# Kernel optimization log

Measured on AMD Instinct MI355X. Metric: run time of the kernel, lower is better.

## Reference

```python
import jax, jax.numpy as jnp
import numpy as np

B, L1, L2, D = 32, 512, 512, 1024


def setup_inputs() -> dict:
    key = jax.random.key(0)
    k1, k2, k3, k4 = jax.random.split(key, 4)
    v1 = jax.random.normal(k1, (B, L1, D), dtype=jnp.float32)
    v2 = jax.random.normal(k2, (B, L2, D), dtype=jnp.float32)
    # row/column is fully masked (which would NaN the softmax).
    v1_mask = jax.random.uniform(k3, (B, L1)) < 0.2
    v2_mask = jax.random.uniform(k4, (B, L2)) < 0.2
    return {"v1": v1, "v2": v2, "v1_mask": v1_mask, "v2_mask": v2_mask}


def reference(v1, v2, v1_mask, v2_mask):
    # similarity: [B, L1, L2]
    sim = jnp.einsum("bid,bjd->bij", v1, v2)
    neg_inf = jnp.float32(-jnp.inf)
    # softmax over v2 positions (dim=2), masking padded v2 columns
    v1_v2_attn = jax.nn.softmax(
        jnp.where(v2_mask[:, None, :], neg_inf, sim), axis=2)
    # softmax over v1 positions (dim=1), masking padded v1 rows
    v2_v1_attn = jax.nn.softmax(
        jnp.where(v1_mask[:, :, None], neg_inf, sim), axis=1)
    attended_v1 = jnp.einsum("bij,bjd->bid", v1_v2_attn, v2)  # [B,L1,D]
    attended_v2 = jnp.einsum("bij,bid->bjd", v2_v1_attn, v1)  # [B,L2,D]
    attended_v1 = jnp.where(v1_mask[:, :, None], 0.0, attended_v1)
    attended_v2 = jnp.where(v2_mask[:, :, None], 0.0, attended_v2)
    return attended_v1, attended_v2
```

## Files before the change

### kernel.cpp

```cpp
#include <hip/hip_runtime.h>
#include <stdint.h>


#define Bn 32
#define Ln 512
#define Dn 1024

typedef __attribute__((ext_vector_type(4))) float f32x4;
typedef __attribute__((ext_vector_type(4))) unsigned short u16x4;
typedef __attribute__((ext_vector_type(8))) unsigned short u16x8;
typedef __attribute__((ext_vector_type(8))) __bf16 bf16x8;

__device__ __forceinline__ unsigned short f2bf(float f) {
  unsigned int u = __float_as_uint(f);
  u += 0x7FFFu + ((u >> 16) & 1u);
  return (unsigned short)(u >> 16);
}

__device__ __forceinline__ void async_cp16(const void* g, void* l) {
  __builtin_amdgcn_global_load_lds(
      (__attribute__((address_space(1))) void*)(g),
      (__attribute__((address_space(3))) void*)(l), 16, 0, 0);
}

__global__ __launch_bounds__(256) void conv_split(
    const float* __restrict__ v1, const float* __restrict__ v2,
    unsigned short* __restrict__ v1t, unsigned short* __restrict__ v2t,
    unsigned short* __restrict__ v1h, unsigned short* __restrict__ v1l,
    unsigned short* __restrict__ v2h, unsigned short* __restrict__ v2l) {
  __shared__ float tile[64][65];
  const int z = blockIdx.z;
  const float* src = (z < Bn) ? v1 : v2;
  unsigned short* dt = (z < Bn) ? v1t : v2t;
  unsigned short* dh = (z < Bn) ? v1h : v2h;
  unsigned short* dl = (z < Bn) ? v1l : v2l;
  const int b = z & 31;
  const int d0 = blockIdx.x << 6;
  const int l0 = blockIdx.y << 6;
  const int tid = threadIdx.x;
  const size_t bo = (size_t)b * Ln * Dn;
#pragma unroll
  for (int it = 0; it < 4; it++) {
    int lin = (it << 8) + tid;
    int l = lin >> 4;
    int d4 = (lin & 15) << 2;
    f32x4 x = *(const f32x4*)(src + (size_t)(b * Ln + l0 + l) * Dn + d0 + d4);
    tile[l][d4] = x[0]; tile[l][d4 + 1] = x[1];
    tile[l][d4 + 2] = x[2]; tile[l][d4 + 3] = x[3];
    u16x4 h4, lo4;
#pragma unroll
    for (int e = 0; e < 4; e++) {
      unsigned int u = __float_as_uint(x[e]);
      h4[e] = (unsigned short)(u >> 16);
      float hf = __uint_as_float(u & 0xFFFF0000u);
      lo4[e] = (unsigned short)(__float_as_uint(x[e] - hf) >> 16);
    }
    int gl = l0 + l;
    int sd = (d0 + d4) ^ (((gl >> 1) & 3) << 3);
    size_t off = bo + (size_t)gl * Dn + sd;
    *(u16x4*)(dh + off) = h4;
    *(u16x4*)(dl + off) = lo4;
  }
  __syncthreads();
#pragma unroll
  for (int it = 0; it < 4; it++) {
    int lin = (it << 8) + tid;
    int d = lin >> 4;
    int l4 = (lin & 15) << 2;
    u16x4 o;
    o[0] = f2bf(tile[l4][d]);     o[1] = f2bf(tile[l4 + 1][d]);
    o[2] = f2bf(tile[l4 + 2][d]); o[3] = f2bf(tile[l4 + 3][d]);
    *(u16x4*)(dt + (size_t)(b * Dn + d0 + d) * Ln + l0 + l4) = o;
  }
}

__global__ __launch_bounds__(256) void sim_gemm(
    const unsigned short* __restrict__ Ahg, const unsigned short* __restrict__ Alg,
    const unsigned short* __restrict__ Bhg, const unsigned short* __restrict__ Blg,
    float* __restrict__ C, const int* __restrict__ v1m,
    const int* __restrict__ v2m,
    float* __restrict__ pmaxR, float* __restrict__ psumR,
    float* __restrict__ pmaxC, float* __restrict__ psumC) {
  __shared__ unsigned short sAh[128 * 32], sAl[128 * 32];
  __shared__ unsigned short sBh[128 * 32], sBl[128 * 32];
  const int b = blockIdx.z;
  const int m0 = blockIdx.y << 7;
  const int n0 = blockIdx.x << 7;
  const int tid = threadIdx.x;
  const int lane = tid & 63;
  const int wave = tid >> 6;
  const int wrow = (wave >> 1) << 6;
  const int wcol = (wave & 1) << 6;
  const int r = lane & 15;
  const int q = lane >> 4;
  const int srow = tid >> 2;
  const int skof = (tid & 3) << 3;
  const size_t bo = (size_t)b * Ln * Dn;
  const unsigned short* gah = Ahg + bo + (size_t)(m0 + srow) * Dn + skof;
  const unsigned short* gal = Alg + bo + (size_t)(m0 + srow) * Dn + skof;
  const unsigned short* gbh = Bhg + bo + (size_t)(n0 + srow) * Dn + skof;
  const unsigned short* gbl = Blg + bo + (size_t)(n0 + srow) * Dn + skof;
  const int ldsw = wave << 9;

  const f32x4 zero4 = {0.f, 0.f, 0.f, 0.f};
  f32x4 acc[4][4];
#pragma unroll
  for (int i = 0; i < 4; i++)
#pragma unroll
    for (int j = 0; j < 4; j++) acc[i][j] = zero4;

  for (int k0 = 0; k0 < Dn; k0 += 32) {
    __syncthreads();
    async_cp16(gah + k0, sAh + ldsw);
    async_cp16(gah + (size_t)64 * Dn + k0, sAh + 2048 + ldsw);
    async_cp16(gal + k0, sAl + ldsw);
    async_cp16(gal + (size_t)64 * Dn + k0, sAl + 2048 + ldsw);
    async_cp16(gbh + k0, sBh + ldsw);
    async_cp16(gbh + (size_t)64 * Dn + k0, sBh + 2048 + ldsw);
    async_cp16(gbl + k0, sBl + ldsw);
    async_cp16(gbl + (size_t)64 * Dn + k0, sBl + 2048 + ldsw);
    __syncthreads();
    bf16x8 ah[4], al[4], bh[4], bl[4];
#pragma unroll
    for (int t = 0; t < 4; t++) {
      int ra = wrow + (t << 4) + r;
      int sa = (ra << 5) + ((q ^ ((ra >> 1) & 3)) << 3);
      ah[t] = *(const bf16x8*)(sAh + sa);
      al[t] = *(const bf16x8*)(sAl + sa);
      int rb = wcol + (t << 4) + r;
      int sb = (rb << 5) + ((q ^ ((rb >> 1) & 3)) << 3);
      bh[t] = *(const bf16x8*)(sBh + sb);
      bl[t] = *(const bf16x8*)(sBl + sb);
    }
#pragma unroll
    for (int tm = 0; tm < 4; tm++)
#pragma unroll
      for (int tn = 0; tn < 4; tn++) {
        acc[tm][tn] = __builtin_amdgcn_mfma_f32_16x16x32_bf16(
            ah[tm], bh[tn], acc[tm][tn], 0, 0, 0);
        acc[tm][tn] = __builtin_amdgcn_mfma_f32_16x16x32_bf16(
            ah[tm], bl[tn], acc[tm][tn], 0, 0, 0);
        acc[tm][tn] = __builtin_amdgcn_mfma_f32_16x16x32_bf16(
            al[tm], bh[tn], acc[tm][tn], 0, 0, 0);
      }
  }

  float* Cb = C + (size_t)b * Ln * Ln;
#pragma unroll
  for (int tm = 0; tm < 4; tm++) {
    int rowb = m0 + wrow + (tm << 4) + (q << 2);
#pragma unroll
    for (int reg = 0; reg < 4; reg++) {
      int row = rowb + reg;
#pragma unroll
      for (int tn = 0; tn < 4; tn++) {
        int col = n0 + wcol + (tn << 4) + r;
        Cb[(size_t)row * Ln + col] = acc[tm][tn][reg];
      }
    }
  }

  const int* mkr = v1m + (b << 9);
  const int* mkc = v2m + (b << 9);
  const float NEGINF = -__builtin_inff();
  unsigned cmb = 0;
#pragma unroll
  for (int tn = 0; tn < 4; tn++)
    cmb |= (mkc[n0 + wcol + (tn << 4) + r] ? 1u : 0u) << tn;
  unsigned rmb = 0;
#pragma unroll
  for (int t2 = 0; t2 < 16; t2++)
    rmb |= (mkr[m0 + wrow + ((t2 >> 2) << 4) + (q << 2) + (t2 & 3)] ? 1u : 0u)
           << t2;

  const int nsub = (n0 + wcol) >> 6;
#pragma unroll
  for (int tm = 0; tm < 4; tm++) {
#pragma unroll
    for (int reg = 0; reg < 4; reg++) {
      float m = NEGINF;
#pragma unroll
      for (int tn = 0; tn < 4; tn++)
        if (!((cmb >> tn) & 1)) m = fmaxf(m, acc[tm][tn][reg]);
#pragma unroll
      for (int off = 1; off < 16; off <<= 1)
        m = fmaxf(m, __shfl_xor(m, off));
      float s = 0.f;
#pragma unroll
      for (int tn = 0; tn < 4; tn++)
        if (!((cmb >> tn) & 1)) s += __expf(acc[tm][tn][reg] - m);
#pragma unroll
      for (int off = 1; off < 16; off <<= 1) s += __shfl_xor(s, off);
      if (r == 0) {
        int row = m0 + wrow + (tm << 4) + (q << 2) + reg;
        int idx = (((b << 3) + nsub) << 9) + row;
        pmaxR[idx] = m;
        psumR[idx] = s;
      }
    }
  }

  const int msub = (m0 + wrow) >> 6;
#pragma unroll
  for (int tn = 0; tn < 4; tn++) {
    float m = NEGINF;
#pragma unroll
    for (int tm = 0; tm < 4; tm++)
#pragma unroll
      for (int reg = 0; reg < 4; reg++)
        if (!((rmb >> ((tm << 2) + reg)) & 1))
          m = fmaxf(m, acc[tm][tn][reg]);
    m = fmaxf(m, __shfl_xor(m, 16));
    m = fmaxf(m, __shfl_xor(m, 32));
    float s = 0.f;
#pragma unroll
    for (int tm = 0; tm < 4; tm++)
#pragma unroll
      for (int reg = 0; reg < 4; reg++)
        if (!((rmb >> ((tm << 2) + reg)) & 1))
          s += __expf(acc[tm][tn][reg] - m);
    s += __shfl_xor(s, 16);
    s += __shfl_xor(s, 32);
    if (q == 0) {
      int col = n0 + wcol + (tn << 4) + r;
      int idx = (((b << 3) + msub) << 9) + col;
      pmaxC[idx] = m;
      psumC[idx] = s;
    }
  }
}

__global__ __launch_bounds__(256) void comb(
    const float* __restrict__ pmaxR, const float* __restrict__ psumR,
    const float* __restrict__ pmaxC, const float* __restrict__ psumC,
    float* __restrict__ rowmax, float* __restrict__ rowrs,
    float* __restrict__ colmax, float* __restrict__ colrs) {
  const int id = (blockIdx.x << 8) + threadIdx.x;
  const int side = id >> 14;
  const int x = id & 16383;
  const float* pm = side ? pmaxC : pmaxR;
  const float* ps = side ? psumC : psumR;
  const int bq = x >> 9;
  const int j = x & 511;
  const float NEGINF = -__builtin_inff();
  float mm[8], sv[8];
#pragma unroll
  for (int p = 0; p < 8; p++) {
    int idx = (((bq << 3) + p) << 9) + j;
    mm[p] = pm[idx];
    sv[p] = ps[idx];
  }
  float M = NEGINF;
#pragma unroll
  for (int p = 0; p < 8; p++) M = fmaxf(M, mm[p]);
  float S = 0.f;
#pragma unroll
  for (int p = 0; p < 8; p++)
    S += (mm[p] > NEGINF) ? sv[p] * __expf(mm[p] - M) : 0.f;
  float rs = 1.f / S;
  if (side) { colmax[x] = M; colrs[x] = rs; }
  else      { rowmax[x] = M; rowrs[x] = rs; }
}

__global__ __launch_bounds__(256) void norm_write(
    const float* __restrict__ sim, const int* __restrict__ v1m,
    const int* __restrict__ v2m,
    const float* __restrict__ rowmax, const float* __restrict__ rowrs,
    const float* __restrict__ colmax, const float* __restrict__ colrs,
    unsigned short* __restrict__ A1, unsigned short* __restrict__ A2t) {
  __shared__ unsigned short Tc[64][66];
  __shared__ float rm[64], rr[64], cmx[64], crx[64];
  const int b = blockIdx.z;
  const int i0 = blockIdx.y << 6;
  const int j0 = blockIdx.x << 6;
  const int tid = threadIdx.x;
  if (tid < 64) {
    cmx[tid] = colmax[(b << 9) + j0 + tid];
    crx[tid] = colrs[(b << 9) + j0 + tid];
  } else if (tid < 128) {
    int t = tid - 64;
    rm[t] = rowmax[(b << 9) + i0 + t];
    rr[t] = rowrs[(b << 9) + i0 + t];
  }
  __syncthreads();
  const int tx = tid & 63;
  const int ty = tid >> 6;
  const float* S = sim + (size_t)b * (Ln * Ln) + j0 + tx;
  const int* mr = v1m + (b << 9) + i0;
  const int jm = v2m[(b << 9) + j0 + tx];
  const float cm0 = cmx[tx];
  const float cs0 = crx[tx];
  unsigned short* A1b = A1 + ((size_t)((b << 9) + i0)) * Ln + j0;
#pragma unroll
  for (int k = 0; k < 16; k++) {
    int il = (k << 2) + ty;
    float x = S[(size_t)(i0 + il) * Ln];
    float e1 = jm ? 0.f : __expf(x - rm[il]) * rr[il];
    A1b[(size_t)il * Ln + tx] = f2bf(e1);
    float e2 = mr[il] ? 0.f : __expf(x - cm0) * cs0;
    Tc[tx][il] = f2bf(e2);
  }
  __syncthreads();
  unsigned short* o = A2t + ((size_t)((b << 9) + j0)) * Ln + i0;
#pragma unroll
  for (int t = 0; t < 4; t++) {
    int c = (t << 8) + tid;
    int j = c >> 4;
    int ch = c & 15;
    u16x4 v;
    v[0] = Tc[j][(ch << 2)];     v[1] = Tc[j][(ch << 2) + 1];
    v[2] = Tc[j][(ch << 2) + 2]; v[3] = Tc[j][(ch << 2) + 3];
    *(u16x4*)(o + (size_t)j * Ln + (ch << 2)) = v;
  }
}

__global__ __launch_bounds__(256) void gemm_nt2(
    const unsigned short* __restrict__ A1g, const unsigned short* __restrict__ A2tg,
    const unsigned short* __restrict__ v2t, const unsigned short* __restrict__ v1t,
    float* __restrict__ out1, float* __restrict__ out2,
    const int* __restrict__ v1m, const int* __restrict__ v2m) {
  const int Mv = 512, Nv = 1024, Kv = 512;
  __shared__ unsigned short As[128 * 32];
  __shared__ unsigned short Bs[128 * 32];
  const int z = blockIdx.z;
  const int b = z & 31;
  const int w2 = z >> 5;
  const unsigned short* A = w2 ? A2tg : A1g;
  const unsigned short* Bm = w2 ? v1t : v2t;
  float* C = w2 ? out2 : out1;
  const int* rowmask = w2 ? v2m : v1m;
  const unsigned short* Ab = A + (size_t)b * Mv * Kv;
  const unsigned short* Bb = Bm + (size_t)b * Nv * Kv;
  float* Cb = C + (size_t)b * Mv * Nv;
  const int m0 = blockIdx.y << 7;
  const int n0 = blockIdx.x << 7;
  const int tid = threadIdx.x;
  const int lane = tid & 63;
  const int wave = tid >> 6;
  const int wrow = (wave >> 1) << 6;
  const int wcol = (wave & 1) << 6;

  const int srow = tid >> 2;
  const int skof = (tid & 3) << 3;
  const unsigned short* ga0 = Ab + (size_t)(m0 + srow) * Kv + skof;
  const unsigned short* ga1 = Ab + (size_t)(m0 + 64 + srow) * Kv + skof;
  const unsigned short* gb0 = Bb + (size_t)(n0 + srow) * Kv + skof;
  const unsigned short* gb1 = Bb + (size_t)(n0 + 64 + srow) * Kv + skof;

  const int r = lane & 15;
  const int q = lane >> 4;

  const f32x4 zero4 = {0.f, 0.f, 0.f, 0.f};
  f32x4 acc[4][4];
#pragma unroll
  for (int i = 0; i < 4; i++)
#pragma unroll
    for (int j = 0; j < 4; j++) acc[i][j] = zero4;

  for (int k0 = 0; k0 < Kv; k0 += 32) {
    __syncthreads();
    async_cp16(ga0 + k0, As + (wave << 9));
    async_cp16(ga1 + k0, As + 2048 + (wave << 9));
    async_cp16(gb0 + k0, Bs + (wave << 9));
    async_cp16(gb1 + k0, Bs + 2048 + (wave << 9));
    __syncthreads();
    bf16x8 af[4], bfr[4];
#pragma unroll
    for (int t = 0; t < 4; t++) {
      af[t] = *(const bf16x8*)(As + ((wrow + (t << 4) + r) << 5) + (q << 3));
      bfr[t] = *(const bf16x8*)(Bs + ((wcol + (t << 4) + r) << 5) + (q << 3));
    }
#pragma unroll
    for (int tm = 0; tm < 4; tm++)
#pragma unroll
      for (int tn = 0; tn < 4; tn++)
        acc[tm][tn] = __builtin_amdgcn_mfma_f32_16x16x32_bf16(
            af[tm], bfr[tn], acc[tm][tn], 0, 0, 0);
  }

  const int* mb = rowmask + b * Mv;
#pragma unroll
  for (int tm = 0; tm < 4; tm++) {
    int rowb = m0 + wrow + (tm << 4) + (q << 2);
#pragma unroll
    for (int reg = 0; reg < 4; reg++) {
      int row = rowb + reg;
      float mz = mb[row] ? 0.f : 1.f;
#pragma unroll
      for (int tn = 0; tn < 4; tn++) {
        int col = n0 + wcol + (tn << 4) + r;
        Cb[(size_t)row * Nv + col] = acc[tm][tn][reg] * mz;
      }
    }
  }
}

extern "C" void kernel_launch(void* const* d_in, const int* in_sizes, int n_in,
                              void* d_out, int out_size, void* d_ws,
                              size_t ws_size, hipStream_t stream) {
  (void)in_sizes; (void)n_in; (void)out_size; (void)ws_size;
  const float* v1 = (const float*)d_in[0];
  const float* v2 = (const float*)d_in[1];
  const int* v1m = (const int*)d_in[2];
  const int* v2m = (const int*)d_in[3];
  float* out1 = (float*)d_out;
  float* out2 = out1 + (size_t)Bn * Ln * Dn;

  char* ws = (char*)d_ws;
  const size_t Mi = 1048576;
  unsigned short* v1t = (unsigned short*)(ws);
  unsigned short* v2t = (unsigned short*)(ws + 32 * Mi);
  unsigned short* v1h = (unsigned short*)(ws + 64 * Mi);
  unsigned short* v2h = (unsigned short*)(ws + 96 * Mi);
  unsigned short* v1l = (unsigned short*)(ws + 128 * Mi);
  unsigned short* v2l = (unsigned short*)(ws + 160 * Mi);
  float* sim = (float*)(ws + 192 * Mi);
  unsigned short* A1 = (unsigned short*)(ws + 64 * Mi);
  unsigned short* A2t = (unsigned short*)(ws + 80 * Mi);
  float* pmaxR = (float*)(ws + 224 * Mi);
  float* psumR = (float*)(ws + 224 * Mi + 512 * 1024);
  float* pmaxC = (float*)(ws + 225 * Mi);
  float* psumC = (float*)(ws + 225 * Mi + 512 * 1024);
  float* rowmax = (float*)(ws + 226 * Mi);
  float* rowrs = (float*)(ws + 226 * Mi + 64 * 1024);
  float* colmax = (float*)(ws + 226 * Mi + 128 * 1024);
  float* colrs = (float*)(ws + 226 * Mi + 192 * 1024);

  dim3 blk(256);
  conv_split<<<dim3(16, 8, 64), blk, 0, stream>>>(v1, v2, v1t, v2t,
                                                  v1h, v1l, v2h, v2l);
  sim_gemm<<<dim3(4, 4, 32), blk, 0, stream>>>(v1h, v1l, v2h, v2l, sim,
                                               v1m, v2m, pmaxR, psumR,
                                               pmaxC, psumC);
  comb<<<dim3(128), blk, 0, stream>>>(pmaxR, psumR, pmaxC, psumC,
                                      rowmax, rowrs, colmax, colrs);
  norm_write<<<dim3(8, 8, 32), blk, 0, stream>>>(sim, v1m, v2m, rowmax, rowrs,
                                                 colmax, colrs, A1, A2t);
  gemm_nt2<<<dim3(8, 4, 64), blk, 0, stream>>>(A1, A2t, v2t, v1t,
                                               out1, out2, v1m, v2m);
}
```

Before: 434.0 us.

## Double-buffer LDS loads in both GEMMs and remap block IDs for XCD locality

```diff
diff --git a/kernel.cpp b/kernel.cpp
--- a/kernel.cpp
+++ b/kernel.cpp
@@ -81,11 +81,13 @@
     const int* __restrict__ v2m,
     float* __restrict__ pmaxR, float* __restrict__ psumR,
     float* __restrict__ pmaxC, float* __restrict__ psumC) {
-  __shared__ unsigned short sAh[128 * 32], sAl[128 * 32];
-  __shared__ unsigned short sBh[128 * 32], sBl[128 * 32];
-  const int b = blockIdx.z;
-  const int m0 = blockIdx.y << 7;
-  const int n0 = blockIdx.x << 7;
+  __shared__ unsigned short sAh[2][4096], sAl[2][4096];
+  __shared__ unsigned short sBh[2][4096], sBl[2][4096];
+  const int bid = blockIdx.x;
+  const int id = ((bid & 7) << 6) + (bid >> 3);
+  const int b = id >> 4;
+  const int m0 = ((id >> 2) & 3) << 7;
+  const int n0 = (id & 3) << 7;
   const int tid = threadIdx.x;
   const int lane = tid & 63;
   const int wave = tid >> 6;
@@ -102,6 +104,18 @@
   const unsigned short* gbl = Blg + bo + (size_t)(n0 + srow) * Dn + skof;
   const int ldsw = wave << 9;
 
+#define SIM_STAGE(nb, kk)                                        \
+  do {                                                           \
+    async_cp16(gah + (kk), &sAh[nb][ldsw]);                      \
+    async_cp16(gah + 64 * Dn + (kk), &sAh[nb][2048 + ldsw]);     \
+    async_cp16(gal + (kk), &sAl[nb][ldsw]);                      \
+    async_cp16(gal + 64 * Dn + (kk), &sAl[nb][2048 + ldsw]);     \
+    async_cp16(gbh + (kk), &sBh[nb][ldsw]);                      \
+    async_cp16(gbh + 64 * Dn + (kk), &sBh[nb][2048 + ldsw]);     \
+    async_cp16(gbl + (kk), &sBl[nb][ldsw]);                      \
+    async_cp16(gbl + 64 * Dn + (kk), &sBl[nb][2048 + ldsw]);     \
+  } while (0)
+
   const f32x4 zero4 = {0.f, 0.f, 0.f, 0.f};
   f32x4 acc[4][4];
 #pragma unroll
@@ -109,28 +123,23 @@
 #pragma unroll
     for (int j = 0; j < 4; j++) acc[i][j] = zero4;
 
-  for (int k0 = 0; k0 < Dn; k0 += 32) {
-    __syncthreads();
-    async_cp16(gah + k0, sAh + ldsw);
-    async_cp16(gah + (size_t)64 * Dn + k0, sAh + 2048 + ldsw);
-    async_cp16(gal + k0, sAl + ldsw);
-    async_cp16(gal + (size_t)64 * Dn + k0, sAl + 2048 + ldsw);
-    async_cp16(gbh + k0, sBh + ldsw);
-    async_cp16(gbh + (size_t)64 * Dn + k0, sBh + 2048 + ldsw);
-    async_cp16(gbl + k0, sBl + ldsw);
-    async_cp16(gbl + (size_t)64 * Dn + k0, sBl + 2048 + ldsw);
-    __syncthreads();
+  SIM_STAGE(0, 0);
+  __syncthreads();
+
+  int cb = 0;
+  for (int k0 = 0; k0 < Dn; k0 += 32, cb ^= 1) {
+    if (k0 + 32 < Dn) SIM_STAGE(cb ^ 1, k0 + 32);
     bf16x8 ah[4], al[4], bh[4], bl[4];
 #pragma unroll
     for (int t = 0; t < 4; t++) {
       int ra = wrow + (t << 4) + r;
       int sa = (ra << 5) + ((q ^ ((ra >> 1) & 3)) << 3);
-      ah[t] = *(const bf16x8*)(sAh + sa);
-      al[t] = *(const bf16x8*)(sAl + sa);
+      ah[t] = *(const bf16x8*)(&sAh[cb][sa]);
+      al[t] = *(const bf16x8*)(&sAl[cb][sa]);
       int rb = wcol + (t << 4) + r;
       int sb = (rb << 5) + ((q ^ ((rb >> 1) & 3)) << 3);
-      bh[t] = *(const bf16x8*)(sBh + sb);
-      bl[t] = *(const bf16x8*)(sBl + sb);
+      bh[t] = *(const bf16x8*)(&sBh[cb][sb]);
+      bl[t] = *(const bf16x8*)(&sBl[cb][sb]);
     }
 #pragma unroll
     for (int tm = 0; tm < 4; tm++)
@@ -143,7 +152,9 @@
         acc[tm][tn] = __builtin_amdgcn_mfma_f32_16x16x32_bf16(
             al[tm], bh[tn], acc[tm][tn], 0, 0, 0);
       }
-  }
+    __syncthreads();
+  }
+#undef SIM_STAGE
 
   float* Cb = C + (size_t)b * Ln * Ln;
 #pragma unroll
@@ -320,9 +331,13 @@
     float* __restrict__ out1, float* __restrict__ out2,
     const int* __restrict__ v1m, const int* __restrict__ v2m) {
   const int Mv = 512, Nv = 1024, Kv = 512;
-  __shared__ unsigned short As[128 * 32];
-  __shared__ unsigned short Bs[128 * 32];
-  const int z = blockIdx.z;
+  __shared__ unsigned short As[2][4096];
+  __shared__ unsigned short Bs[2][4096];
+  const int bid = blockIdx.x;
+  const int id = ((bid & 7) << 8) + (bid >> 3);
+  const int z = id >> 5;
+  const int m0 = ((id >> 3) & 3) << 7;
+  const int n0 = (id & 7) << 7;
   const int b = z & 31;
   const int w2 = z >> 5;
   const unsigned short* A = w2 ? A2tg : A1g;
@@ -332,8 +347,6 @@
   const unsigned short* Ab = A + (size_t)b * Mv * Kv;
   const unsigned short* Bb = Bm + (size_t)b * Nv * Kv;
   float* Cb = C + (size_t)b * Mv * Nv;
-  const int m0 = blockIdx.y << 7;
-  const int n0 = blockIdx.x << 7;
   const int tid = threadIdx.x;
   const int lane = tid & 63;
   const int wave = tid >> 6;
@@ -346,6 +359,15 @@
   const unsigned short* ga1 = Ab + (size_t)(m0 + 64 + srow) * Kv + skof;
   const unsigned short* gb0 = Bb + (size_t)(n0 + srow) * Kv + skof;
   const unsigned short* gb1 = Bb + (size_t)(n0 + 64 + srow) * Kv + skof;
+  const int ldsw = wave << 9;
+
+#define PV_STAGE(nb, kk)                            \
+  do {                                              \
+    async_cp16(ga0 + (kk), &As[nb][ldsw]);          \
+    async_cp16(ga1 + (kk), &As[nb][2048 + ldsw]);   \
+    async_cp16(gb0 + (kk), &Bs[nb][ldsw]);          \
+    async_cp16(gb1 + (kk), &Bs[nb][2048 + ldsw]);   \
+  } while (0)
 
   const int r = lane & 15;
   const int q = lane >> 4;
@@ -357,18 +379,17 @@
 #pragma unroll
     for (int j = 0; j < 4; j++) acc[i][j] = zero4;
 
-  for (int k0 = 0; k0 < Kv; k0 += 32) {
-    __syncthreads();
-    async_cp16(ga0 + k0, As + (wave << 9));
-    async_cp16(ga1 + k0, As + 2048 + (wave << 9));
-    async_cp16(gb0 + k0, Bs + (wave << 9));
-    async_cp16(gb1 + k0, Bs + 2048 + (wave << 9));
-    __syncthreads();
+  PV_STAGE(0, 0);
+  __syncthreads();
+
+  int cb = 0;
+  for (int k0 = 0; k0 < Kv; k0 += 32, cb ^= 1) {
+    if (k0 + 32 < Kv) PV_STAGE(cb ^ 1, k0 + 32);
     bf16x8 af[4], bfr[4];
 #pragma unroll
     for (int t = 0; t < 4; t++) {
-      af[t] = *(const bf16x8*)(As + ((wrow + (t << 4) + r) << 5) + (q << 3));
-      bfr[t] = *(const bf16x8*)(Bs + ((wcol + (t << 4) + r) << 5) + (q << 3));
+      af[t] = *(const bf16x8*)(&As[cb][((wrow + (t << 4) + r) << 5) + (q << 3)]);
+      bfr[t] = *(const bf16x8*)(&Bs[cb][((wcol + (t << 4) + r) << 5) + (q << 3)]);
     }
 #pragma unroll
     for (int tm = 0; tm < 4; tm++)
@@ -376,7 +397,9 @@
       for (int tn = 0; tn < 4; tn++)
         acc[tm][tn] = __builtin_amdgcn_mfma_f32_16x16x32_bf16(
             af[tm], bfr[tn], acc[tm][tn], 0, 0, 0);
-  }
+    __syncthreads();
+  }
+#undef PV_STAGE
 
   const int* mb = rowmask + b * Mv;
 #pragma unroll
@@ -429,13 +452,13 @@
   dim3 blk(256);
   conv_split<<<dim3(16, 8, 64), blk, 0, stream>>>(v1, v2, v1t, v2t,
                                                   v1h, v1l, v2h, v2l);
-  sim_gemm<<<dim3(4, 4, 32), blk, 0, stream>>>(v1h, v1l, v2h, v2l, sim,
-                                               v1m, v2m, pmaxR, psumR,
-                                               pmaxC, psumC);
+  sim_gemm<<<dim3(512), blk, 0, stream>>>(v1h, v1l, v2h, v2l, sim,
+                                          v1m, v2m, pmaxR, psumR,
+                                          pmaxC, psumC);
   comb<<<dim3(128), blk, 0, stream>>>(pmaxR, psumR, pmaxC, psumC,
                                       rowmax, rowrs, colmax, colrs);
   norm_write<<<dim3(8, 8, 32), blk, 0, stream>>>(sim, v1m, v2m, rowmax, rowrs,
                                                  colmax, colrs, A1, A2t);
-  gemm_nt2<<<dim3(8, 4, 64), blk, 0, stream>>>(A1, A2t, v2t, v1t,
-                                               out1, out2, v1m, v2m);
-}
+  gemm_nt2<<<dim3(2048), blk, 0, stream>>>(A1, A2t, v2t, v1t,
+                                           out1, out2, v1m, v2m);
+}
```

New measurement: 411.5 us. -5.2%, faster.
